# Kernel tuning notes

Hardware: AMD Instinct MI355X
Metric: run time of the kernel (lower is better)

## Reference

```python
import jax, jax.numpy as jnp
import numpy as np

B = 131072      # tokens routed (e.g., 16 seqs x 8192 tokens)
D_MODEL = 768
N_EXPERTS = 8
TOP_K = 2


def setup_inputs() -> dict:
    key = jax.random.key(0)
    k_h, k_w, k_b = jax.random.split(key, 3)
    h = jax.random.normal(k_h, (B, D_MODEL), dtype=jnp.float32)
    gate_w = jax.random.normal(k_w, (N_EXPERTS, D_MODEL), dtype=jnp.float32) * 0.02
    gate_b = jax.random.normal(k_b, (N_EXPERTS,), dtype=jnp.float32) * 0.02
    return {"h": h, "gate_w": gate_w, "gate_b": gate_b}


def reference(h, gate_w, gate_b):
    # gate projection: [B, d_model] @ [d_model, n_experts] + bias -> [B, n_experts]
    logits = jnp.einsum("bd,ed->be", h, gate_w) + gate_b
    # top-k selection (values, indices), then softmax over the top-k logits
    topk_vals, topk_idx = jax.lax.top_k(logits, TOP_K)   # [B, top_k] each
    weights = jax.nn.softmax(topk_vals, axis=-1)          # [B, top_k]
    return (topk_idx, weights)
```

## Files before the change

### kernel.cpp

```cpp
#include <hip/hip_runtime.h>
#include <hip/hip_bf16.h>


#define B_TOKENS 131072
#define DM 768
#define NE 8
#define TAU 2.5e-4f
#define NEG_BIG -3.0e38f

typedef __attribute__((ext_vector_type(8))) short bf16x8;
typedef __attribute__((ext_vector_type(4))) float f32x4;

__device__ __forceinline__ unsigned short f32_to_bf16(float f) {
    __hip_bfloat16 b = __float2bfloat16(f);
    return *reinterpret_cast<unsigned short*>(&b);
}
__device__ __forceinline__ float bf16_to_f32(unsigned short u) {
    return __uint_as_float((unsigned)u << 16);
}

__global__ __launch_bounds__(256) void router_main(
    const float* __restrict__ h,
    const float* __restrict__ gw,
    const float* __restrict__ gb,
    float* __restrict__ out,
    unsigned char* __restrict__ flags)
{
    __shared__ __align__(16) unsigned short w_lds[24 * 576 + 8];

    const int tid  = threadIdx.x;
    const int lane = tid & 63;
    const int wv   = tid >> 6;
    const int col  = lane & 15;
    const int kg   = lane >> 4;

    for (int idx = tid; idx < NE * DM; idx += 256) {
        const int e = idx / DM, k = idx - e * DM;
        const float w = gw[idx];
        const unsigned short hb = f32_to_bf16(w);
        const unsigned short lb = f32_to_bf16(w - bf16_to_f32(hb));
        const int ks = k >> 5, kk = k & 31;
        const int phys = (((kk & 15) >> 2) << 3) + (kk & 3) + ((kk & 16) ? 4 : 0);
        w_lds[ks * 576 + e * 72 + phys]      = hb;
        w_lds[ks * 576 + e * 72 + 32 + phys] = lb;
    }
    if (tid < 8) w_lds[24 * 576 + tid] = 0;

    const float bias_lane = (col < 8) ? gb[col] : NEG_BIG;
    __syncthreads();

    const int tile0 = (blockIdx.x * 4 + wv) * 2;
    const float* arow0 = h + (size_t)(tile0 * 16 + col) * DM + kg * 4;
    const float* arow1 = arow0 + (size_t)16 * DM;

    const unsigned short* bptr =
        (col < 8) ? &w_lds[col * 72 + kg * 8] : &w_lds[24 * 576];
    const int bstep = (col < 8) ? 576 : 0;
    const int bloff = (col < 8) ? 32 : 0;

    f32x4 acc0 = {0.f, 0.f, 0.f, 0.f};
    f32x4 acc1 = {0.f, 0.f, 0.f, 0.f};

#pragma unroll 2
    for (int ks = 0; ks < 24; ++ks) {
        const float4 p0 = *reinterpret_cast<const float4*>(arow0 + ks * 32);
        const float4 q0 = *reinterpret_cast<const float4*>(arow0 + ks * 32 + 16);
        const float4 p1 = *reinterpret_cast<const float4*>(arow1 + ks * 32);
        const float4 q1 = *reinterpret_cast<const float4*>(arow1 + ks * 32 + 16);

        const bf16x8 bhi = *reinterpret_cast<const bf16x8*>(bptr + ks * bstep);
        const bf16x8 blo = *reinterpret_cast<const bf16x8*>(bptr + ks * bstep + bloff);

        bf16x8 ahi0, alo0, ahi1, alo1;
        {
            const float f0[8] = {p0.x, p0.y, p0.z, p0.w, q0.x, q0.y, q0.z, q0.w};
            const float f1[8] = {p1.x, p1.y, p1.z, p1.w, q1.x, q1.y, q1.z, q1.w};
#pragma unroll
            for (int j = 0; j < 8; ++j) {
                unsigned short hb = f32_to_bf16(f0[j]);
                ahi0[j] = (short)hb;
                alo0[j] = (short)f32_to_bf16(f0[j] - bf16_to_f32(hb));
                hb = f32_to_bf16(f1[j]);
                ahi1[j] = (short)hb;
                alo1[j] = (short)f32_to_bf16(f1[j] - bf16_to_f32(hb));
            }
        }
        acc0 = __builtin_amdgcn_mfma_f32_16x16x32_bf16(ahi0, bhi, acc0, 0, 0, 0);
        acc0 = __builtin_amdgcn_mfma_f32_16x16x32_bf16(ahi0, blo, acc0, 0, 0, 0);
        acc0 = __builtin_amdgcn_mfma_f32_16x16x32_bf16(alo0, bhi, acc0, 0, 0, 0);
        acc1 = __builtin_amdgcn_mfma_f32_16x16x32_bf16(ahi1, bhi, acc1, 0, 0, 0);
        acc1 = __builtin_amdgcn_mfma_f32_16x16x32_bf16(ahi1, blo, acc1, 0, 0, 0);
        acc1 = __builtin_amdgcn_mfma_f32_16x16x32_bf16(alo1, bhi, acc1, 0, 0, 0);
    }

    const unsigned gsh = (unsigned)(lane & 48);

    auto epi = [&](const f32x4& acc, int tile) {
#pragma unroll
        for (int i = 0; i < 4; ++i) {
            const float lg = acc[i] + bias_lane;
            float a0 = lg, a1 = NEG_BIG, a2 = NEG_BIG;
#pragma unroll
            for (int m = 1; m <= 4; m <<= 1) {
                const float b0 = __shfl_xor(a0, m);
                const float b1 = __shfl_xor(a1, m);
                const float b2 = __shfl_xor(a2, m);
                const float x  = fminf(a0, b0);
                const float c0 = fmaxf(a0, b0);
                const float y  = fmaxf(a1, b1);
                const float z  = fminf(a1, b1);
                const float c1 = fmaxf(x, y);
                const float c2 = fmaxf(fminf(x, y), fmaxf(z, fmaxf(a2, b2)));
                a0 = c0; a1 = c1; a2 = c2;
            }
            const unsigned long long m0 = __ballot(lg == a0);
            const unsigned long long m1 = __ballot(lg == a1);
            const unsigned mk0 = (unsigned)(m0 >> gsh) & 0xFFu;
            const unsigned mk1 = (unsigned)(m1 >> gsh) & 0xFFu;
            const int i0 = __builtin_ctz(mk0);
            const unsigned rest = mk0 & (mk0 - 1);
            const int i1 = (a1 == a0) ? __builtin_ctz(rest | 0x100u)
                                      : __builtin_ctz(mk1 | 0x100u);

            const bool amb = (a0 - a1 < TAU) || (a1 - a2 < TAU);
            const float ex = expf(a1 - a0);
            const float w1 = ex / (1.f + ex);
            const float w0 = 1.f - w1;

            if (col == 0) {
                const size_t t = (size_t)(tile * 16 + (lane >> 4) * 4 + i);
                *reinterpret_cast<float2*>(&out[2 * t]) =
                    make_float2((float)i0, (float)i1);
                *reinterpret_cast<float2*>(&out[2 * (size_t)B_TOKENS + 2 * t]) =
                    make_float2(w0, w1);
                flags[t] = amb ? 1 : 0;
            }
        }
    };
    epi(acc0, tile0);
    epi(acc1, tile0 + 1);
}

__global__ __launch_bounds__(256) void router_repair(
    const float* __restrict__ h,
    const float* __restrict__ gw,
    const float* __restrict__ gb,
    float* __restrict__ out,
    const unsigned char* __restrict__ flags)
{
    const int lane = threadIdx.x & 63;
    const int w = (blockIdx.x * blockDim.x + threadIdx.x) >> 6;
    const int t0 = w * 64;
    if (t0 >= B_TOKENS) return;

    const unsigned char f = flags[t0 + lane];
    unsigned long long mask = __ballot(f != 0);
    if (mask == 0ull) return;

    float wf[NE][3][4];
#pragma unroll
    for (int e = 0; e < NE; ++e)
#pragma unroll
        for (int g = 0; g < 3; ++g) {
            const float4 vv = *reinterpret_cast<const float4*>(
                &gw[e * DM + g * 256 + lane * 4]);
            wf[e][g][0] = vv.x; wf[e][g][1] = vv.y;
            wf[e][g][2] = vv.z; wf[e][g][3] = vv.w;
        }
    double biasd[NE];
#pragma unroll
    for (int e = 0; e < NE; ++e) biasd[e] = (double)gb[e];

    const bool hi32 = (lane & 32) != 0;
    const bool hi16 = (lane & 16) != 0;
    const bool hi8  = (lane & 8)  != 0;

    while (mask) {
        const int p = __ffsll((unsigned long long)mask) - 1;
        mask &= (mask - 1);
        const int t = t0 + p;

        const float* hr = h + (size_t)t * DM;
        float4 buf[3];
#pragma unroll
        for (int g = 0; g < 3; ++g)
            buf[g] = *reinterpret_cast<const float4*>(&hr[g * 256 + lane * 4]);

        double acc[NE] = {0, 0, 0, 0, 0, 0, 0, 0};
#pragma unroll
        for (int g = 0; g < 3; ++g) {
            const float* bp = reinterpret_cast<const float*>(&buf[g]);
#pragma unroll
            for (int j = 0; j < 4; ++j) {
                const double hd = (double)bp[j];
#pragma unroll
                for (int e = 0; e < NE; ++e)
                    acc[e] = fma(hd, (double)wf[e][g][j], acc[e]);
            }
        }
        double d4[4];
#pragma unroll
        for (int j = 0; j < 4; ++j) {
            const double give = hi32 ? acc[j] : acc[4 + j];
            const double keep = hi32 ? acc[4 + j] : acc[j];
            d4[j] = keep + __shfl_xor(give, 32);
        }
        double d2[2];
#pragma unroll
        for (int j = 0; j < 2; ++j) {
            const double give = hi16 ? d4[j] : d4[2 + j];
            const double keep = hi16 ? d4[2 + j] : d4[j];
            d2[j] = keep + __shfl_xor(give, 16);
        }
        const double give = hi8 ? d2[0] : d2[1];
        const double keep = hi8 ? d2[1] : d2[0];
        double dv = keep + __shfl_xor(give, 8);
        dv += __shfl_xor(dv, 4);
        dv += __shfl_xor(dv, 2);
        dv += __shfl_xor(dv, 1);

        double dlg[NE];
#pragma unroll
        for (int e = 0; e < NE; ++e)
            dlg[e] = __shfl(dv, (e << 3) | (lane & 7)) + biasd[e];

        int i0 = 0; double dv0 = dlg[0];
#pragma unroll
        for (int e = 1; e < NE; ++e)
            if (dlg[e] > dv0) { dv0 = dlg[e]; i0 = e; }
        int i1 = (i0 == 0) ? 1 : 0; double dv1 = dlg[i1];
#pragma unroll
        for (int e = 0; e < NE; ++e)
            if (e != i0 && dlg[e] > dv1) { dv1 = dlg[e]; i1 = e; }

        const float ex = expf((float)(dv1 - dv0));
        const float w1 = ex / (1.0f + ex);
        const float w0 = 1.0f - w1;

        if (lane == 0) {
            *reinterpret_cast<float2*>(&out[2 * (size_t)t]) =
                make_float2((float)i0, (float)i1);
            *reinterpret_cast<float2*>(
                &out[2 * (size_t)B_TOKENS + 2 * (size_t)t]) =
                make_float2(w0, w1);
        }
    }
}

extern "C" void kernel_launch(void* const* d_in, const int* in_sizes, int n_in,
                              void* d_out, int out_size, void* d_ws, size_t ws_size,
                              hipStream_t stream) {
    const float* h  = (const float*)d_in[0];
    const float* gw = (const float*)d_in[1];
    const float* gb = (const float*)d_in[2];
    float* out = (float*)d_out;
    unsigned char* flags = (unsigned char*)d_ws;

    router_main<<<dim3(1024), dim3(256), 0, stream>>>(h, gw, gb, out, flags);
    router_repair<<<dim3(512), dim3(256), 0, stream>>>(h, gw, gb, out, flags);
}
```

Before: 86.53 us.

## Fuse ambiguous-token fp64 repair into main router kernel, drop flags buffer

The separate repair kernel and the per-token flag array are removed. Each wave now builds a bitmask of ambiguous tokens through a ballot in the epilogue and recomputes those tokens in fp64 inline, reading the gate weights from global memory. Unambiguous tokens are written directly. This saves a second launch, the flags writes and the repair kernel's scan over all flags. In exchange, waves that hit ambiguous tokens serialize the fp64 work inside the main kernel, and the weights are re-read per token.

Measured after the change: 98.24 us. 1.14x slower.

```diff
diff --git a/kernel.cpp b/kernel.cpp
--- a/kernel.cpp
+++ b/kernel.cpp
@@ -19,12 +19,11 @@
     return __uint_as_float((unsigned)u << 16);
 }
 
-__global__ __launch_bounds__(256) void router_main(
+__global__ __launch_bounds__(256) void router_fused(
     const float* __restrict__ h,
     const float* __restrict__ gw,
     const float* __restrict__ gb,
-    float* __restrict__ out,
-    unsigned char* __restrict__ flags)
+    float* __restrict__ out)
 {
     __shared__ __align__(16) unsigned short w_lds[24 * 576 + 8];
 
@@ -94,8 +93,9 @@
     }
 
     const unsigned gsh = (unsigned)(lane & 48);
-
-    auto epi = [&](const f32x4& acc, int tile) {
+    unsigned wavemask = 0;
+
+    auto epi = [&](const f32x4& acc, int tile, int tsel) {
 #pragma unroll
         for (int i = 0; i < 4; ++i) {
             const float lg = acc[i] + bias_lane;
@@ -123,126 +123,105 @@
                                       : __builtin_ctz(mk1 | 0x100u);
 
             const bool amb = (a0 - a1 < TAU) || (a1 - a2 < TAU);
+
+            const unsigned long long ab = __ballot((col == 0) && amb);
+            const unsigned base = (unsigned)(tsel * 16 + i);
+            wavemask |= ((unsigned)(ab >> 0)  & 1u) << (base + 0);
+            wavemask |= ((unsigned)(ab >> 16) & 1u) << (base + 4);
+            wavemask |= ((unsigned)(ab >> 32) & 1u) << (base + 8);
+            wavemask |= ((unsigned)(ab >> 48) & 1u) << (base + 12);
+
             const float ex = expf(a1 - a0);
             const float w1 = ex / (1.f + ex);
             const float w0 = 1.f - w1;
 
-            if (col == 0) {
+            if (col == 0 && !amb) {
                 const size_t t = (size_t)(tile * 16 + (lane >> 4) * 4 + i);
                 *reinterpret_cast<float2*>(&out[2 * t]) =
                     make_float2((float)i0, (float)i1);
                 *reinterpret_cast<float2*>(&out[2 * (size_t)B_TOKENS + 2 * t]) =
                     make_float2(w0, w1);
-                flags[t] = amb ? 1 : 0;
             }
         }
     };
-    epi(acc0, tile0);
-    epi(acc1, tile0 + 1);
-}
-
-__global__ __launch_bounds__(256) void router_repair(
-    const float* __restrict__ h,
-    const float* __restrict__ gw,
-    const float* __restrict__ gb,
-    float* __restrict__ out,
-    const unsigned char* __restrict__ flags)
-{
-    const int lane = threadIdx.x & 63;
-    const int w = (blockIdx.x * blockDim.x + threadIdx.x) >> 6;
-    const int t0 = w * 64;
-    if (t0 >= B_TOKENS) return;
-
-    const unsigned char f = flags[t0 + lane];
-    unsigned long long mask = __ballot(f != 0);
-    if (mask == 0ull) return;
-
-    float wf[NE][3][4];
-#pragma unroll
-    for (int e = 0; e < NE; ++e)
-#pragma unroll
-        for (int g = 0; g < 3; ++g) {
-            const float4 vv = *reinterpret_cast<const float4*>(
-                &gw[e * DM + g * 256 + lane * 4]);
-            wf[e][g][0] = vv.x; wf[e][g][1] = vv.y;
-            wf[e][g][2] = vv.z; wf[e][g][3] = vv.w;
-        }
-    double biasd[NE];
-#pragma unroll
-    for (int e = 0; e < NE; ++e) biasd[e] = (double)gb[e];
-
-    const bool hi32 = (lane & 32) != 0;
-    const bool hi16 = (lane & 16) != 0;
-    const bool hi8  = (lane & 8)  != 0;
-
-    while (mask) {
-        const int p = __ffsll((unsigned long long)mask) - 1;
-        mask &= (mask - 1);
-        const int t = t0 + p;
-
-        const float* hr = h + (size_t)t * DM;
-        float4 buf[3];
-#pragma unroll
-        for (int g = 0; g < 3; ++g)
-            buf[g] = *reinterpret_cast<const float4*>(&hr[g * 256 + lane * 4]);
-
-        double acc[NE] = {0, 0, 0, 0, 0, 0, 0, 0};
-#pragma unroll
-        for (int g = 0; g < 3; ++g) {
-            const float* bp = reinterpret_cast<const float*>(&buf[g]);
+    epi(acc0, tile0, 0);
+    epi(acc1, tile0 + 1, 1);
+
+    if (__builtin_expect(wavemask != 0, 0)) {
+        const bool hi32 = (lane & 32) != 0;
+        const bool hi16 = (lane & 16) != 0;
+        const bool hi8  = (lane & 8)  != 0;
+        while (wavemask) {
+            const int p = __builtin_ctz(wavemask);
+            wavemask &= wavemask - 1;
+            const int t = tile0 * 16 + p;
+
+            const float* hr = h + (size_t)t * DM;
+            float4 buf[3];
+#pragma unroll
+            for (int g = 0; g < 3; ++g)
+                buf[g] = *reinterpret_cast<const float4*>(&hr[g * 256 + lane * 4]);
+
+            double acc[NE] = {0, 0, 0, 0, 0, 0, 0, 0};
+#pragma unroll
+            for (int g = 0; g < 3; ++g) {
+                const float* bp = reinterpret_cast<const float*>(&buf[g]);
+#pragma unroll
+                for (int e = 0; e < NE; ++e) {
+                    const float4 wv4 = *reinterpret_cast<const float4*>(
+                        &gw[e * DM + g * 256 + lane * 4]);
+                    acc[e] = fma((double)bp[0], (double)wv4.x, acc[e]);
+                    acc[e] = fma((double)bp[1], (double)wv4.y, acc[e]);
+                    acc[e] = fma((double)bp[2], (double)wv4.z, acc[e]);
+                    acc[e] = fma((double)bp[3], (double)wv4.w, acc[e]);
+                }
+            }
+            double d4[4];
 #pragma unroll
             for (int j = 0; j < 4; ++j) {
-                const double hd = (double)bp[j];
-#pragma unroll
-                for (int e = 0; e < NE; ++e)
-                    acc[e] = fma(hd, (double)wf[e][g][j], acc[e]);
-            }
-        }
-        double d4[4];
-#pragma unroll
-        for (int j = 0; j < 4; ++j) {
-            const double give = hi32 ? acc[j] : acc[4 + j];
-            const double keep = hi32 ? acc[4 + j] : acc[j];
-            d4[j] = keep + __shfl_xor(give, 32);
-        }
-        double d2[2];
-#pragma unroll
-        for (int j = 0; j < 2; ++j) {
-            const double give = hi16 ? d4[j] : d4[2 + j];
-            const double keep = hi16 ? d4[2 + j] : d4[j];
-            d2[j] = keep + __shfl_xor(give, 16);
-        }
-        const double give = hi8 ? d2[0] : d2[1];
-        const double keep = hi8 ? d2[1] : d2[0];
-        double dv = keep + __shfl_xor(give, 8);
-        dv += __shfl_xor(dv, 4);
-        dv += __shfl_xor(dv, 2);
-        dv += __shfl_xor(dv, 1);
-
-        double dlg[NE];
-#pragma unroll
-        for (int e = 0; e < NE; ++e)
-            dlg[e] = __shfl(dv, (e << 3) | (lane & 7)) + biasd[e];
-
-        int i0 = 0; double dv0 = dlg[0];
-#pragma unroll
-        for (int e = 1; e < NE; ++e)
-            if (dlg[e] > dv0) { dv0 = dlg[e]; i0 = e; }
-        int i1 = (i0 == 0) ? 1 : 0; double dv1 = dlg[i1];
-#pragma unroll
-        for (int e = 0; e < NE; ++e)
-            if (e != i0 && dlg[e] > dv1) { dv1 = dlg[e]; i1 = e; }
-
-        const float ex = expf((float)(dv1 - dv0));
-        const float w1 = ex / (1.0f + ex);
-        const float w0 = 1.0f - w1;
-
-        if (lane == 0) {
-            *reinterpret_cast<float2*>(&out[2 * (size_t)t]) =
-                make_float2((float)i0, (float)i1);
-            *reinterpret_cast<float2*>(
-                &out[2 * (size_t)B_TOKENS + 2 * (size_t)t]) =
-                make_float2(w0, w1);
+                const double give = hi32 ? acc[j] : acc[4 + j];
+                const double keep = hi32 ? acc[4 + j] : acc[j];
+                d4[j] = keep + __shfl_xor(give, 32);
+            }
+            double d2[2];
+#pragma unroll
+            for (int j = 0; j < 2; ++j) {
+                const double give = hi16 ? d4[j] : d4[2 + j];
+                const double keep = hi16 ? d4[2 + j] : d4[j];
+                d2[j] = keep + __shfl_xor(give, 16);
+            }
+            const double give = hi8 ? d2[0] : d2[1];
+            const double keep = hi8 ? d2[1] : d2[0];
+            double dv = keep + __shfl_xor(give, 8);
+            dv += __shfl_xor(dv, 4);
+            dv += __shfl_xor(dv, 2);
+            dv += __shfl_xor(dv, 1);
+
+            double dlg[NE];
+#pragma unroll
+            for (int e = 0; e < NE; ++e)
+                dlg[e] = __shfl(dv, (e << 3) | (lane & 7)) + (double)gb[e];
+
+            int i0 = 0; double dv0 = dlg[0];
+#pragma unroll
+            for (int e = 1; e < NE; ++e)
+                if (dlg[e] > dv0) { dv0 = dlg[e]; i0 = e; }
+            int i1 = (i0 == 0) ? 1 : 0; double dv1 = dlg[i1];
+#pragma unroll
+            for (int e = 0; e < NE; ++e)
+                if (e != i0 && dlg[e] > dv1) { dv1 = dlg[e]; i1 = e; }
+
+            const float ex = expf((float)(dv1 - dv0));
+            const float w1 = ex / (1.0f + ex);
+            const float w0 = 1.0f - w1;
+
+            if (lane == 0) {
+                *reinterpret_cast<float2*>(&out[2 * (size_t)t]) =
+                    make_float2((float)i0, (float)i1);
+                *reinterpret_cast<float2*>(
+                    &out[2 * (size_t)B_TOKENS + 2 * (size_t)t]) =
+                    make_float2(w0, w1);
+            }
         }
     }
 }
@@ -254,8 +233,6 @@
     const float* gw = (const float*)d_in[1];
     const float* gb = (const float*)d_in[2];
     float* out = (float*)d_out;
-    unsigned char* flags = (unsigned char*)d_ws;
-
-    router_main<<<dim3(1024), dim3(256), 0, stream>>>(h, gw, gb, out, flags);
-    router_repair<<<dim3(512), dim3(256), 0, stream>>>(h, gw, gb, out, flags);
-}
+
+    router_fused<<<dim3(1024), dim3(256), 0, stream>>>(h, gw, gb, out);
+}
```
